# Kernel tuning notes

Measured on AMD Instinct MI355X. Metric: run time of the kernel, lower is better.

The kernel has to match this reference:

```python
import jax, jax.numpy as jnp
import numpy as np
import math

B, L, D, H = 2, 2048, 2048, 16
DK = D // H  # 128

def _rope_tables(dim, max_len, base=10000.0):
    freqs = 1.0 / (base ** (np.arange(0, dim, 2, dtype=np.float32) / dim))
    t = np.arange(max_len, dtype=np.float32)
    ang = np.outer(t, freqs)  # [max_len, dim//2]
    return jnp.asarray(np.cos(ang)), jnp.asarray(np.sin(ang))

def setup_inputs() -> dict:
    key = jax.random.key(0)
    kx, kq, ko = jax.random.split(key, 3)
    x = jax.random.normal(kx, (B, L, D), dtype=jnp.float32)
    w_qkv = jax.random.normal(kq, (D, 3 * D), dtype=jnp.float32) * 0.02
    w_o = jax.random.normal(ko, (D, D), dtype=jnp.float32) * 0.02
    cos, sin = _rope_tables(DK, L)
    return {"x": x, "w_qkv": w_qkv, "w_o": w_o, "cos": cos, "sin": sin}

def _apply_rope(t, cos, sin):
    # t: [B, H, L, DK]; cos/sin: [L, DK//2]
    d2 = t.shape[-1] // 2
    t1, t2 = t[..., :d2], t[..., d2:]
    c = cos[None, None, :, :]
    s = sin[None, None, :, :]
    return jnp.concatenate([t1 * c - t2 * s, t1 * s + t2 * c], axis=-1)

def reference(x, w_qkv, w_o, cos, sin):
    b, l, d = x.shape
    qkv = (x @ w_qkv).reshape(b, l, 3, H, DK)
    q = jnp.transpose(qkv[:, :, 0], (0, 2, 1, 3))  # [B,H,L,DK]
    k = jnp.transpose(qkv[:, :, 1], (0, 2, 1, 3))
    v = jnp.transpose(qkv[:, :, 2], (0, 2, 1, 3))
    q = _apply_rope(q, cos[:l], sin[:l])
    k = _apply_rope(k, cos[:l], sin[:l])
    scores = jnp.einsum('bhqd,bhkd->bhqk', q, k) / math.sqrt(DK)
    causal = jnp.triu(jnp.ones((l, l), dtype=bool), k=1)  # total_len - L + 1 = 1
    scores = jnp.where(causal[None, None], -jnp.inf, scores)
    attn = jax.nn.softmax(scores, axis=-1)  # dropout p=0 -> identity
    out = jnp.einsum('bhqk,bhkd->bhqd', attn, v)
    out = jnp.transpose(out, (0, 2, 1, 3)).reshape(b, l, d)
    return out @ w_o, k, v
```

## Files before the change

### kernel.cpp

```cpp
#include <hip/hip_runtime.h>
#include <hip/hip_bf16.h>

#define NB 2
#define NL 2048
#define ND 2048
#define NH 16
#define NDK 128
#define SCALE2 0.12753102866606474f

#define AS1 __attribute__((address_space(1)))
#define AS3 __attribute__((address_space(3)))

typedef __attribute__((ext_vector_type(8))) __bf16 bf16x8;
typedef __attribute__((ext_vector_type(4))) float f32x4;

__device__ __forceinline__ unsigned short f2bf(float f) {
    union { float f; unsigned u; } v; v.f = f;
    return (unsigned short)((v.u + 0x7fffu + ((v.u >> 16) & 1u)) >> 16);
}
__device__ __forceinline__ float bf2f(unsigned short h) {
    union { unsigned u; float f; } v; v.u = ((unsigned)h) << 16;
    return v.f;
}

__global__ __launch_bounds__(256)
void convert_bf16_kernel(const float* __restrict__ in, unsigned short* __restrict__ outp)
{
    int i = blockIdx.x * 256 + threadIdx.x;
    const float4 a = ((const float4*)in)[2 * i];
    const float4 b = ((const float4*)in)[2 * i + 1];
    unsigned short t[8] = { f2bf(a.x), f2bf(a.y), f2bf(a.z), f2bf(a.w),
                            f2bf(b.x), f2bf(b.y), f2bf(b.z), f2bf(b.w) };
    ((uint4*)outp)[i] = *(uint4*)t;
}

__global__ __launch_bounds__(256)
void transpose_convert_kernel(const float* __restrict__ in, unsigned short* __restrict__ outp,
                              int R, int C)
{
    __shared__ float T[64][65];
    const int tr0 = blockIdx.y * 64;
    const int tc0 = blockIdx.x * 64;
    const int t = threadIdx.x;
    const int r = t >> 2;
    const int q = t & 3;
    const float* src = in + (size_t)(tr0 + r) * C + tc0 + q * 16;
    #pragma unroll
    for (int i = 0; i < 4; i++) {
        float4 f = *(const float4*)(src + 4 * i);
        T[r][q * 16 + 4 * i + 0] = f.x;
        T[r][q * 16 + 4 * i + 1] = f.y;
        T[r][q * 16 + 4 * i + 2] = f.z;
        T[r][q * 16 + 4 * i + 3] = f.w;
    }
    __syncthreads();
    unsigned short tmp[16];
    #pragma unroll
    for (int i = 0; i < 16; i++) tmp[i] = f2bf(T[q * 16 + i][r]);
    unsigned short* dst = outp + (size_t)(tc0 + r) * R + tr0 + q * 16;
    *(uint4*)dst       = *(uint4*)&tmp[0];
    *(uint4*)(dst + 8) = *(uint4*)&tmp[8];
}

__global__ __launch_bounds__(256)
void transpose_v_kernel(const float* __restrict__ v, unsigned short* __restrict__ vt)
{
    __shared__ float T[64][65];
    const int bh = blockIdx.z;
    const int l0 = blockIdx.y * 64;
    const int d0 = blockIdx.x * 64;
    const int t = threadIdx.x;
    const int r = t >> 2;
    const int q = t & 3;
    const float* src = v + (size_t)bh * NL * NDK + (size_t)(l0 + r) * NDK + d0 + q * 16;
    #pragma unroll
    for (int i = 0; i < 4; i++) {
        float4 f = *(const float4*)(src + 4 * i);
        T[r][q * 16 + 4 * i + 0] = f.x;
        T[r][q * 16 + 4 * i + 1] = f.y;
        T[r][q * 16 + 4 * i + 2] = f.z;
        T[r][q * 16 + 4 * i + 3] = f.w;
    }
    __syncthreads();
    unsigned short tmp[16];
    #pragma unroll
    for (int i = 0; i < 16; i++) tmp[i] = f2bf(T[q * 16 + i][r]);
    unsigned short* dst = vt + (size_t)bh * NDK * NL + (size_t)(d0 + r) * NL + l0 + q * 16;
    *(uint4*)dst       = *(uint4*)&tmp[0];
    *(uint4*)(dst + 8) = *(uint4*)&tmp[8];
}

template<int EPI>
__global__ __launch_bounds__(256)
void gemm_bf16(const unsigned short* __restrict__ A, const unsigned short* __restrict__ Bt,
               float* __restrict__ y_dst,
               unsigned short* __restrict__ q_raw,
               float* __restrict__ k_dst, float* __restrict__ v_dst,
               int K, int NT)
{
    __shared__ __align__(16) unsigned short As[3][128][32];
    __shared__ __align__(16) unsigned short Bs[3][128][32];

    const int tid = threadIdx.x;
    const int lane = tid & 63;
    const int l16 = lane & 15, g = lane >> 4;
    const int w = tid >> 6;
    const int wr = w >> 1, wc = w & 1;

    const int cpn = NT >> 3;
    const int bid = blockIdx.x;
    const int xcd = bid & 7, local = bid >> 3;
    const int bx = xcd * cpn + local % cpn;
    const int by = local / cpn;
    const int m0 = by * 128, n0 = bx * 128;

    const int rowl = (w << 4) + (lane >> 2);
    const int swl = (rowl >> 1) & 3;
    const int kofl = ((lane & 3) ^ swl) << 3;
    const unsigned short* gA = A + (size_t)(m0 + rowl) * K + kofl;
    const unsigned short* gB = Bt + (size_t)(n0 + rowl) * K + kofl;
    const int ldsoff = (w << 10) + (lane << 4);

    f32x4 acc[4][4] = {};
    const int NTILES = K >> 5;

    auto STAGE = [&](int t, int buf) {
        const int k0 = t << 5;
        char* baseA = (char*)&As[buf][0][0] + ldsoff;
        char* baseB = (char*)&Bs[buf][0][0] + ldsoff;
        #pragma unroll
        for (int i = 0; i < 2; i++) {
            __builtin_amdgcn_global_load_lds((const AS1 void*)(gA + (size_t)i * 64 * K + k0),
                                             (AS3 void*)(baseA + i * 4096), 16, 0, 0);
            __builtin_amdgcn_global_load_lds((const AS1 void*)(gB + (size_t)i * 64 * K + k0),
                                             (AS3 void*)(baseB + i * 4096), 16, 0, 0);
        }
    };

    const int rsw = (l16 >> 1) & 3;

    STAGE(0, 0); STAGE(1, 1);

    int bufC = 0;
    for (int t = 0; t < NTILES; t++) {
        const int bufS = (bufC == 0) ? 2 : bufC - 1;
        if (t + 2 < NTILES) STAGE(t + 2, bufS);
        if (t + 2 < NTILES)      asm volatile("s_waitcnt vmcnt(8)" ::: "memory");
        else if (t + 1 < NTILES) asm volatile("s_waitcnt vmcnt(4)" ::: "memory");
        else                     asm volatile("s_waitcnt vmcnt(0)" ::: "memory");
        __builtin_amdgcn_s_barrier();
        __builtin_amdgcn_sched_barrier(0);

        const char* pa = (const char*)&As[bufC][0][0];
        const char* pb = (const char*)&Bs[bufC][0][0];
        bf16x8 af[4], bfr[4];
        #pragma unroll
        for (int r = 0; r < 4; r++) {
            int row = wr * 64 + r * 16 + l16;
            af[r] = *(const bf16x8*)(pa + row * 64 + ((g ^ rsw) << 4));
        }
        #pragma unroll
        for (int c = 0; c < 4; c++) {
            int row = wc * 64 + c * 16 + l16;
            bfr[c] = *(const bf16x8*)(pb + row * 64 + ((g ^ rsw) << 4));
        }
        #pragma unroll
        for (int r = 0; r < 4; r++)
            #pragma unroll
            for (int c = 0; c < 4; c++)
                acc[r][c] = __builtin_amdgcn_mfma_f32_16x16x32_bf16(af[r], bfr[c], acc[r][c], 0, 0, 0);

        __builtin_amdgcn_s_barrier();
        __builtin_amdgcn_sched_barrier(0);
        bufC = (bufC == 2) ? 0 : bufC + 1;
    }

    if constexpr (EPI == 0) {
        const int m3 = bx >> 4, h = bx & 15;
        #pragma unroll
        for (int r = 0; r < 4; r++) {
            int mrow = m0 + wr * 64 + r * 16 + g * 4;
            int b = mrow >> 11, l = mrow & 2047;
            size_t rb = ((size_t)(b * NH + h) * NL + l) * NDK;
            #pragma unroll
            for (int c = 0; c < 4; c++) {
                int dk = wc * 64 + c * 16 + l16;
                #pragma unroll
                for (int i = 0; i < 4; i++) {
                    float val = acc[r][c][i];
                    size_t off = rb + (size_t)i * NDK + dk;
                    if (m3 == 0) q_raw[off] = f2bf(val);
                    else if (m3 == 1) k_dst[off] = val;
                    else v_dst[off] = val;
                }
            }
        }
    } else {
        #pragma unroll
        for (int r = 0; r < 4; r++) {
            int mrow = m0 + wr * 64 + r * 16 + g * 4;
            #pragma unroll
            for (int c = 0; c < 4; c++) {
                int ncol = n0 + wc * 64 + c * 16 + l16;
                #pragma unroll
                for (int i = 0; i < 4; i++)
                    y_dst[(size_t)(mrow + i) * ND + ncol] = acc[r][c][i];
            }
        }
    }
}

__global__ __launch_bounds__(256)
void rope_k_kernel(float* __restrict__ kp, unsigned short* __restrict__ k_bf,
                   const float* __restrict__ ct, const float* __restrict__ st)
{
    int idx = blockIdx.x * 256 + threadIdx.x;
    int d = (idx & 15) << 2;
    int rr = idx >> 4;
    size_t ro = (size_t)rr * NDK;
    int l = rr & (NL - 1);
    float4 c  = *(const float4*)(ct + l * 64 + d);
    float4 s  = *(const float4*)(st + l * 64 + d);
    float4 t1 = *(const float4*)(kp + ro + d);
    float4 t2 = *(const float4*)(kp + ro + d + 64);
    float4 o1, o2;
    o1.x = t1.x * c.x - t2.x * s.x;  o2.x = t1.x * s.x + t2.x * c.x;
    o1.y = t1.y * c.y - t2.y * s.y;  o2.y = t1.y * s.y + t2.y * c.y;
    o1.z = t1.z * c.z - t2.z * s.z;  o2.z = t1.z * s.z + t2.z * c.z;
    o1.w = t1.w * c.w - t2.w * s.w;  o2.w = t1.w * s.w + t2.w * c.w;
    *(float4*)(kp + ro + d)      = o1;
    *(float4*)(kp + ro + d + 64) = o2;
    unsigned short u1[4] = { f2bf(o1.x), f2bf(o1.y), f2bf(o1.z), f2bf(o1.w) };
    unsigned short u2[4] = { f2bf(o2.x), f2bf(o2.y), f2bf(o2.z), f2bf(o2.w) };
    *(uint2*)(k_bf + ro + d)      = *(uint2*)u1;
    *(uint2*)(k_bf + ro + d + 64) = *(uint2*)u2;
}

__global__ __launch_bounds__(256)
void attn_kernel(const unsigned short* __restrict__ q,
                 const unsigned short* __restrict__ k,
                 const unsigned short* __restrict__ vt,
                 unsigned short* __restrict__ attn_out,
                 const float* __restrict__ ct, const float* __restrict__ st)
{
    __shared__ __align__(16) unsigned short Ks[64][128];
    __shared__ __align__(16) unsigned short Vts[128][64];
    __shared__ __align__(16) unsigned short Ps[4][16][64];

    char* const ksb = (char*)&Ks[0][0];
    char* const vsb = (char*)&Vts[0][0];
    char* const psb = (char*)&Ps[0][0][0];

    const int tid = threadIdx.x, lane = tid & 63, w = tid >> 6;
    const int l16 = lane & 15, g = lane >> 4;
    const int bh = blockIdx.x;
    const int b = bh >> 4, h = bh & 15;
    const size_t base = (size_t)bh * NL * NDK;

    const int krow = tid >> 2;
    const int kq = tid & 3;
    const int kwb = krow * 256 + kq * 64;
    const int kwx = (krow & 7) << 4;
    const int vrow = tid >> 1;
    const int vh = tid & 1;
    const int vwb = vrow * 128 + vh * 64;
    const int vwx = (vrow & 7) << 4;

    const int rdx = (l16 & 7) << 4;

    const unsigned short* const kbase = k + base + (size_t)krow * NDK + kq * 32;
    const unsigned short* const vbase = vt + base + (size_t)vrow * NL + vh * 32;

    const int jq = 31 - (int)blockIdx.y;
    const int qb = jq * 64;

    bf16x8 aq[4];
    {
        const int l = qb + w * 16 + l16;
        const unsigned short* src = q + base + (size_t)l * NDK + g * 8;
        union { bf16x8 v; unsigned short s[8]; } raw[4], outv[4];
        #pragma unroll
        for (int ks2 = 0; ks2 < 4; ks2++) raw[ks2].v = *(const bf16x8*)(src + ks2 * 32);
        const float* cb = ct + (size_t)l * 64 + g * 8;
        const float* sb = st + (size_t)l * 64 + g * 8;
        float cv[2][8], sv2[2][8];
        #pragma unroll
        for (int hh = 0; hh < 2; hh++) {
            float4 c0 = *(const float4*)(cb + 32 * hh);
            float4 c1 = *(const float4*)(cb + 32 * hh + 4);
            float4 s0 = *(const float4*)(sb + 32 * hh);
            float4 s1 = *(const float4*)(sb + 32 * hh + 4);
            cv[hh][0]=c0.x; cv[hh][1]=c0.y; cv[hh][2]=c0.z; cv[hh][3]=c0.w;
            cv[hh][4]=c1.x; cv[hh][5]=c1.y; cv[hh][6]=c1.z; cv[hh][7]=c1.w;
            sv2[hh][0]=s0.x; sv2[hh][1]=s0.y; sv2[hh][2]=s0.z; sv2[hh][3]=s0.w;
            sv2[hh][4]=s1.x; sv2[hh][5]=s1.y; sv2[hh][6]=s1.z; sv2[hh][7]=s1.w;
        }
        #pragma unroll
        for (int hh = 0; hh < 2; hh++)
            #pragma unroll
            for (int j = 0; j < 8; j++) {
                float t1 = bf2f(raw[hh].s[j]), t2 = bf2f(raw[hh + 2].s[j]);
                float c = cv[hh][j], s = sv2[hh][j];
                outv[hh].s[j]     = f2bf(t1 * c - t2 * s);
                outv[hh + 2].s[j] = f2bf(t1 * s + t2 * c);
            }
        #pragma unroll
        for (int ks2 = 0; ks2 < 4; ks2++) aq[ks2] = outv[ks2].v;
    }

    f32x4 o[8] = {};
    float m_r[4], lv[4];
    #pragma unroll
    for (int i = 0; i < 4; i++) { m_r[i] = -1e30f; lv[i] = 0.f; }

    uint4 pk0, pk1, pk2, pk3, pv0, pv1, pv2, pv3;
    {
        const unsigned short* ks = kbase;
        pk0 = *(const uint4*)(ks);
        pk1 = *(const uint4*)(ks + 8);
        pk2 = *(const uint4*)(ks + 16);
        pk3 = *(const uint4*)(ks + 24);
        const unsigned short* vs = vbase;
        pv0 = *(const uint4*)(vs);
        pv1 = *(const uint4*)(vs + 8);
        pv2 = *(const uint4*)(vs + 16);
        pv3 = *(const uint4*)(vs + 24);
    }

    for (int kv0 = 0; kv0 <= qb; kv0 += 64) {
        __syncthreads();
        *(uint4*)(ksb + ((kwb     ) ^ kwx)) = pk0;
        *(uint4*)(ksb + ((kwb + 16) ^ kwx)) = pk1;
        *(uint4*)(ksb + ((kwb + 32) ^ kwx)) = pk2;
        *(uint4*)(ksb + ((kwb + 48) ^ kwx)) = pk3;
        *(uint4*)(vsb + ((vwb     ) ^ vwx)) = pv0;
        *(uint4*)(vsb + ((vwb + 16) ^ vwx)) = pv1;
        *(uint4*)(vsb + ((vwb + 32) ^ vwx)) = pv2;
        *(uint4*)(vsb + ((vwb + 48) ^ vwx)) = pv3;
        __syncthreads();

        if (kv0 + 64 <= qb) {
            const unsigned short* ks = kbase + (size_t)(kv0 + 64) * NDK;
            pk0 = *(const uint4*)(ks);
            pk1 = *(const uint4*)(ks + 8);
            pk2 = *(const uint4*)(ks + 16);
            pk3 = *(const uint4*)(ks + 24);
            const unsigned short* vs = vbase + kv0 + 64;
            pv0 = *(const uint4*)(vs);
            pv1 = *(const uint4*)(vs + 8);
            pv2 = *(const uint4*)(vs + 16);
            pv3 = *(const uint4*)(vs + 24);
            __builtin_amdgcn_sched_barrier(0);
        }

        f32x4 sv[4];
        __builtin_amdgcn_s_setprio(1);
        #pragma unroll
        for (int cf = 0; cf < 4; cf++) {
            const int krb = (cf * 16 + l16) * 256 + g * 16;
            f32x4 a = {};
            #pragma unroll
            for (int ks2 = 0; ks2 < 4; ks2++) {
                bf16x8 kf = *(const bf16x8*)(ksb + ((krb + 64 * ks2) ^ rdx));
                a = __builtin_amdgcn_mfma_f32_16x16x32_bf16(aq[ks2], kf, a, 0, 0, 0);
            }
            sv[cf] = a;
        }
        __builtin_amdgcn_s_setprio(0);

        const int kvl = kv0 + l16;
        const int rowb = qb + w * 16 + g * 4;
        #pragma unroll
        for (int i = 0; i < 4; i++) {
            int row = rowb + i;
            float s0 = sv[0][i] * SCALE2;
            float s1 = sv[1][i] * SCALE2;
            float s2 = sv[2][i] * SCALE2;
            float s3 = sv[3][i] * SCALE2;
            if (kvl      > row) s0 = -1e30f;
            if (kvl + 16 > row) s1 = -1e30f;
            if (kvl + 32 > row) s2 = -1e30f;
            if (kvl + 48 > row) s3 = -1e30f;
            float mx = fmaxf(fmaxf(s0, s1), fmaxf(s2, s3));
            mx = fmaxf(mx, __shfl_xor(mx, 1));
            mx = fmaxf(mx, __shfl_xor(mx, 2));
            mx = fmaxf(mx, __shfl_xor(mx, 4));
            mx = fmaxf(mx, __shfl_xor(mx, 8));
            float mnew = fmaxf(m_r[i], mx);
            float fac = exp2f(m_r[i] - mnew);
            float p0 = exp2f(s0 - mnew);
            float p1 = exp2f(s1 - mnew);
            float p2 = exp2f(s2 - mnew);
            float p3 = exp2f(s3 - mnew);
            lv[i] = lv[i] * fac + ((p0 + p1) + (p2 + p3));
            m_r[i] = mnew;
            #pragma unroll
            for (int c8 = 0; c8 < 8; c8++) o[c8][i] *= fac;
            const int pr = g * 4 + i;
            char* pw = psb + w * 2048 + pr * 128;
            const int px = (pr & 7) << 4;
            const int cb2 = l16 << 1;
            *(unsigned short*)(pw + ((cb2)      ^ px)) = f2bf(p0);
            *(unsigned short*)(pw + ((cb2 + 32) ^ px)) = f2bf(p1);
            *(unsigned short*)(pw + ((cb2 + 64) ^ px)) = f2bf(p2);
            *(unsigned short*)(pw + ((cb2 + 96) ^ px)) = f2bf(p3);
        }
        asm volatile("s_waitcnt lgkmcnt(0)" ::: "memory");
        __builtin_amdgcn_sched_barrier(0);

        bf16x8 pf[2];
        #pragma unroll
        for (int kc = 0; kc < 2; kc++)
            pf[kc] = *(const bf16x8*)(psb + w * 2048 + l16 * 128 + ((kc * 64 + g * 16) ^ rdx));
        __builtin_amdgcn_s_setprio(1);
        #pragma unroll
        for (int c8 = 0; c8 < 8; c8++) {
            const int vrb = (c8 * 16 + l16) * 128 + g * 16;
            #pragma unroll
            for (int kc = 0; kc < 2; kc++) {
                bf16x8 vf = *(const bf16x8*)(vsb + ((vrb + kc * 64) ^ rdx));
                o[c8] = __builtin_amdgcn_mfma_f32_16x16x32_bf16(pf[kc], vf, o[c8], 0, 0, 0);
            }
        }
        __builtin_amdgcn_s_setprio(0);
    }

    #pragma unroll
    for (int i = 0; i < 4; i++) {
        float ls = lv[i];
        ls += __shfl_xor(ls, 1);
        ls += __shfl_xor(ls, 2);
        ls += __shfl_xor(ls, 4);
        ls += __shfl_xor(ls, 8);
        float inv = 1.0f / ls;
        int qrow = qb + w * 16 + g * 4 + i;
        size_t rb = ((size_t)(b * NL + qrow)) * ND + h * NDK;
        #pragma unroll
        for (int c8 = 0; c8 < 8; c8++)
            attn_out[rb + c8 * 16 + l16] = f2bf(o[c8][i] * inv);
    }
}

__global__ void ws_signature_kernel(float* y) { if (threadIdx.x == 0) y[0] = 12345.0f; }

extern "C" void kernel_launch(void* const* d_in, const int* in_sizes, int n_in,
                              void* d_out, int out_size, void* d_ws, size_t ws_size,
                              hipStream_t stream)
{
    const float* x     = (const float*)d_in[0];
    const float* w_qkv = (const float*)d_in[1];
    const float* w_o   = (const float*)d_in[2];
    const float* ct    = (const float*)d_in[3];
    const float* st    = (const float*)d_in[4];

    const size_t NTOK = (size_t)NB * NL * ND;
    float* y_out = (float*)d_out;
    float* k_out = y_out + NTOK;
    float* v_out = y_out + 2 * NTOK;

    const size_t need = (6 * NTOK + 4 * (size_t)ND * ND) * sizeof(unsigned short);
    if (ws_size < need) {
        ws_signature_kernel<<<1, 64, 0, stream>>>(y_out);
        return;
    }
    unsigned short* x_bf  = (unsigned short*)d_ws;
    unsigned short* Wt    = x_bf + NTOK;
    unsigned short* Wt_o  = Wt + (size_t)3 * ND * ND;
    unsigned short* q_raw = Wt_o + (size_t)ND * ND;
    unsigned short* q_bf  = q_raw + NTOK;
    unsigned short* k_bf  = q_bf + NTOK;
    unsigned short* Vt    = k_bf + NTOK;
    unsigned short* a_bf  = Vt + NTOK;

    convert_bf16_kernel<<<4096, 256, 0, stream>>>(x, x_bf);
    transpose_convert_kernel<<<dim3(96, 32), 256, 0, stream>>>(w_qkv, Wt, ND, 3 * ND);
    transpose_convert_kernel<<<dim3(32, 32), 256, 0, stream>>>(w_o, Wt_o, ND, ND);
    gemm_bf16<0><<<1536, 256, 0, stream>>>(x_bf, Wt, nullptr, q_raw, k_out, v_out, ND, 48);
    rope_k_kernel<<<4096, 256, 0, stream>>>(k_out, k_bf, ct, st);
    transpose_v_kernel<<<dim3(2, 32, 32), 256, 0, stream>>>(v_out, Vt);
    attn_kernel<<<dim3(32, 32), 256, 0, stream>>>(q_raw, k_bf, Vt, a_bf, ct, st);
    gemm_bf16<1><<<512, 256, 0, stream>>>(a_bf, Wt_o, y_out, nullptr, nullptr, nullptr, ND, 16);
}
```

Before: 329.4 us.

## Merge prep and mid kernels; pair causal query tiles per attention block

The three preprocessing kernels (x conversion and both weight transposes) become one launch that dispatches on block index, and the rope-K and V-transpose kernels are merged the same way. The attention grid is halved, and each block now handles two query tiles, a long one (31-y) and a short one (y), so every block does about the same amount of causal work. This removes launch overhead and tail imbalance in attention, at the cost of fewer concurrent blocks and a serial two-phase loop per block.

```diff
diff --git a/kernel.cpp b/kernel.cpp
--- a/kernel.cpp
+++ b/kernel.cpp
@@ -23,27 +23,15 @@
     return v.f;
 }
 
-__global__ __launch_bounds__(256)
-void convert_bf16_kernel(const float* __restrict__ in, unsigned short* __restrict__ outp)
-{
-    int i = blockIdx.x * 256 + threadIdx.x;
-    const float4 a = ((const float4*)in)[2 * i];
-    const float4 b = ((const float4*)in)[2 * i + 1];
-    unsigned short t[8] = { f2bf(a.x), f2bf(a.y), f2bf(a.z), f2bf(a.w),
-                            f2bf(b.x), f2bf(b.y), f2bf(b.z), f2bf(b.w) };
-    ((uint4*)outp)[i] = *(uint4*)t;
-}
-
-__global__ __launch_bounds__(256)
-void transpose_convert_kernel(const float* __restrict__ in, unsigned short* __restrict__ outp,
-                              int R, int C)
+__device__ __forceinline__ void transpose_tile(const float* __restrict__ in,
+                                               unsigned short* __restrict__ outp,
+                                               int R, int C, int bx, int by, int tid)
 {
     __shared__ float T[64][65];
-    const int tr0 = blockIdx.y * 64;
-    const int tc0 = blockIdx.x * 64;
-    const int t = threadIdx.x;
-    const int r = t >> 2;
-    const int q = t & 3;
+    const int tr0 = by * 64;
+    const int tc0 = bx * 64;
+    const int r = tid >> 2;
+    const int q = tid & 3;
     const float* src = in + (size_t)(tr0 + r) * C + tc0 + q * 16;
     #pragma unroll
     for (int i = 0; i < 4; i++) {
@@ -63,31 +51,26 @@
 }
 
 __global__ __launch_bounds__(256)
-void transpose_v_kernel(const float* __restrict__ v, unsigned short* __restrict__ vt)
-{
-    __shared__ float T[64][65];
-    const int bh = blockIdx.z;
-    const int l0 = blockIdx.y * 64;
-    const int d0 = blockIdx.x * 64;
-    const int t = threadIdx.x;
-    const int r = t >> 2;
-    const int q = t & 3;
-    const float* src = v + (size_t)bh * NL * NDK + (size_t)(l0 + r) * NDK + d0 + q * 16;
-    #pragma unroll
-    for (int i = 0; i < 4; i++) {
-        float4 f = *(const float4*)(src + 4 * i);
-        T[r][q * 16 + 4 * i + 0] = f.x;
-        T[r][q * 16 + 4 * i + 1] = f.y;
-        T[r][q * 16 + 4 * i + 2] = f.z;
-        T[r][q * 16 + 4 * i + 3] = f.w;
-    }
-    __syncthreads();
-    unsigned short tmp[16];
-    #pragma unroll
-    for (int i = 0; i < 16; i++) tmp[i] = f2bf(T[q * 16 + i][r]);
-    unsigned short* dst = vt + (size_t)bh * NDK * NL + (size_t)(d0 + r) * NL + l0 + q * 16;
-    *(uint4*)dst       = *(uint4*)&tmp[0];
-    *(uint4*)(dst + 8) = *(uint4*)&tmp[8];
+void prep_kernel(const float* __restrict__ x, unsigned short* __restrict__ x_bf,
+                 const float* __restrict__ w_qkv, unsigned short* __restrict__ Wt,
+                 const float* __restrict__ w_o, unsigned short* __restrict__ Wt_o)
+{
+    const int bid = blockIdx.x;
+    const int tid = threadIdx.x;
+    if (bid < 4096) {
+        int i = bid * 256 + tid;
+        const float4 a = ((const float4*)x)[2 * i];
+        const float4 b = ((const float4*)x)[2 * i + 1];
+        unsigned short t[8] = { f2bf(a.x), f2bf(a.y), f2bf(a.z), f2bf(a.w),
+                                f2bf(b.x), f2bf(b.y), f2bf(b.z), f2bf(b.w) };
+        ((uint4*)x_bf)[i] = *(uint4*)t;
+    } else if (bid < 7168) {
+        int b2 = bid - 4096;
+        transpose_tile(w_qkv, Wt, ND, 3 * ND, b2 % 96, b2 / 96, tid);
+    } else {
+        int b3 = bid - 7168;
+        transpose_tile(w_o, Wt_o, ND, ND, b3 & 31, b3 >> 5, tid);
+    }
 }
 
 template<int EPI>
@@ -211,29 +194,58 @@
 }
 
 __global__ __launch_bounds__(256)
-void rope_k_kernel(float* __restrict__ kp, unsigned short* __restrict__ k_bf,
-                   const float* __restrict__ ct, const float* __restrict__ st)
-{
-    int idx = blockIdx.x * 256 + threadIdx.x;
-    int d = (idx & 15) << 2;
-    int rr = idx >> 4;
-    size_t ro = (size_t)rr * NDK;
-    int l = rr & (NL - 1);
-    float4 c  = *(const float4*)(ct + l * 64 + d);
-    float4 s  = *(const float4*)(st + l * 64 + d);
-    float4 t1 = *(const float4*)(kp + ro + d);
-    float4 t2 = *(const float4*)(kp + ro + d + 64);
-    float4 o1, o2;
-    o1.x = t1.x * c.x - t2.x * s.x;  o2.x = t1.x * s.x + t2.x * c.x;
-    o1.y = t1.y * c.y - t2.y * s.y;  o2.y = t1.y * s.y + t2.y * c.y;
-    o1.z = t1.z * c.z - t2.z * s.z;  o2.z = t1.z * s.z + t2.z * c.z;
-    o1.w = t1.w * c.w - t2.w * s.w;  o2.w = t1.w * s.w + t2.w * c.w;
-    *(float4*)(kp + ro + d)      = o1;
-    *(float4*)(kp + ro + d + 64) = o2;
-    unsigned short u1[4] = { f2bf(o1.x), f2bf(o1.y), f2bf(o1.z), f2bf(o1.w) };
-    unsigned short u2[4] = { f2bf(o2.x), f2bf(o2.y), f2bf(o2.z), f2bf(o2.w) };
-    *(uint2*)(k_bf + ro + d)      = *(uint2*)u1;
-    *(uint2*)(k_bf + ro + d + 64) = *(uint2*)u2;
+void mid_kernel(float* __restrict__ kp, unsigned short* __restrict__ k_bf,
+                const float* __restrict__ ct, const float* __restrict__ st,
+                const float* __restrict__ v, unsigned short* __restrict__ vt)
+{
+    const int bid = blockIdx.x;
+    const int tid = threadIdx.x;
+    if (bid < 4096) {
+        int idx = bid * 256 + tid;
+        int d = (idx & 15) << 2;
+        int rr = idx >> 4;
+        size_t ro = (size_t)rr * NDK;
+        int l = rr & (NL - 1);
+        float4 c  = *(const float4*)(ct + l * 64 + d);
+        float4 s  = *(const float4*)(st + l * 64 + d);
+        float4 t1 = *(const float4*)(kp + ro + d);
+        float4 t2 = *(const float4*)(kp + ro + d + 64);
+        float4 o1, o2;
+        o1.x = t1.x * c.x - t2.x * s.x;  o2.x = t1.x * s.x + t2.x * c.x;
+        o1.y = t1.y * c.y - t2.y * s.y;  o2.y = t1.y * s.y + t2.y * c.y;
+        o1.z = t1.z * c.z - t2.z * s.z;  o2.z = t1.z * s.z + t2.z * c.z;
+        o1.w = t1.w * c.w - t2.w * s.w;  o2.w = t1.w * s.w + t2.w * c.w;
+        *(float4*)(kp + ro + d)      = o1;
+        *(float4*)(kp + ro + d + 64) = o2;
+        unsigned short u1[4] = { f2bf(o1.x), f2bf(o1.y), f2bf(o1.z), f2bf(o1.w) };
+        unsigned short u2[4] = { f2bf(o2.x), f2bf(o2.y), f2bf(o2.z), f2bf(o2.w) };
+        *(uint2*)(k_bf + ro + d)      = *(uint2*)u1;
+        *(uint2*)(k_bf + ro + d + 64) = *(uint2*)u2;
+    } else {
+        __shared__ float T[64][65];
+        int b2 = bid - 4096;
+        const int bh = b2 >> 6;
+        const int l0 = ((b2 >> 1) & 31) * 64;
+        const int d0 = (b2 & 1) * 64;
+        const int r = tid >> 2;
+        const int q = tid & 3;
+        const float* src = v + (size_t)bh * NL * NDK + (size_t)(l0 + r) * NDK + d0 + q * 16;
+        #pragma unroll
+        for (int i = 0; i < 4; i++) {
+            float4 f = *(const float4*)(src + 4 * i);
+            T[r][q * 16 + 4 * i + 0] = f.x;
+            T[r][q * 16 + 4 * i + 1] = f.y;
+            T[r][q * 16 + 4 * i + 2] = f.z;
+            T[r][q * 16 + 4 * i + 3] = f.w;
+        }
+        __syncthreads();
+        unsigned short tmp[16];
+        #pragma unroll
+        for (int i = 0; i < 16; i++) tmp[i] = f2bf(T[q * 16 + i][r]);
+        unsigned short* dst = vt + (size_t)bh * NDK * NL + (size_t)(d0 + r) * NL + l0 + q * 16;
+        *(uint4*)dst       = *(uint4*)&tmp[0];
+        *(uint4*)(dst + 8) = *(uint4*)&tmp[8];
+    }
 }
 
 __global__ __launch_bounds__(256)
@@ -271,173 +283,175 @@
     const unsigned short* const kbase = k + base + (size_t)krow * NDK + kq * 32;
     const unsigned short* const vbase = vt + base + (size_t)vrow * NL + vh * 32;
 
-    const int jq = 31 - (int)blockIdx.y;
-    const int qb = jq * 64;
-
-    bf16x8 aq[4];
-    {
-        const int l = qb + w * 16 + l16;
-        const unsigned short* src = q + base + (size_t)l * NDK + g * 8;
-        union { bf16x8 v; unsigned short s[8]; } raw[4], outv[4];
-        #pragma unroll
-        for (int ks2 = 0; ks2 < 4; ks2++) raw[ks2].v = *(const bf16x8*)(src + ks2 * 32);
-        const float* cb = ct + (size_t)l * 64 + g * 8;
-        const float* sb = st + (size_t)l * 64 + g * 8;
-        float cv[2][8], sv2[2][8];
-        #pragma unroll
-        for (int hh = 0; hh < 2; hh++) {
-            float4 c0 = *(const float4*)(cb + 32 * hh);
-            float4 c1 = *(const float4*)(cb + 32 * hh + 4);
-            float4 s0 = *(const float4*)(sb + 32 * hh);
-            float4 s1 = *(const float4*)(sb + 32 * hh + 4);
-            cv[hh][0]=c0.x; cv[hh][1]=c0.y; cv[hh][2]=c0.z; cv[hh][3]=c0.w;
-            cv[hh][4]=c1.x; cv[hh][5]=c1.y; cv[hh][6]=c1.z; cv[hh][7]=c1.w;
-            sv2[hh][0]=s0.x; sv2[hh][1]=s0.y; sv2[hh][2]=s0.z; sv2[hh][3]=s0.w;
-            sv2[hh][4]=s1.x; sv2[hh][5]=s1.y; sv2[hh][6]=s1.z; sv2[hh][7]=s1.w;
-        }
-        #pragma unroll
-        for (int hh = 0; hh < 2; hh++)
-            #pragma unroll
-            for (int j = 0; j < 8; j++) {
-                float t1 = bf2f(raw[hh].s[j]), t2 = bf2f(raw[hh + 2].s[j]);
-                float c = cv[hh][j], s = sv2[hh][j];
-                outv[hh].s[j]     = f2bf(t1 * c - t2 * s);
-                outv[hh + 2].s[j] = f2bf(t1 * s + t2 * c);
-            }
-        #pragma unroll
-        for (int ks2 = 0; ks2 < 4; ks2++) aq[ks2] = outv[ks2].v;
-    }
-
-    f32x4 o[8] = {};
-    float m_r[4], lv[4];
-    #pragma unroll
-    for (int i = 0; i < 4; i++) { m_r[i] = -1e30f; lv[i] = 0.f; }
-
-    uint4 pk0, pk1, pk2, pk3, pv0, pv1, pv2, pv3;
-    {
-        const unsigned short* ks = kbase;
-        pk0 = *(const uint4*)(ks);
-        pk1 = *(const uint4*)(ks + 8);
-        pk2 = *(const uint4*)(ks + 16);
-        pk3 = *(const uint4*)(ks + 24);
-        const unsigned short* vs = vbase;
-        pv0 = *(const uint4*)(vs);
-        pv1 = *(const uint4*)(vs + 8);
-        pv2 = *(const uint4*)(vs + 16);
-        pv3 = *(const uint4*)(vs + 24);
-    }
-
-    for (int kv0 = 0; kv0 <= qb; kv0 += 64) {
-        __syncthreads();
-        *(uint4*)(ksb + ((kwb     ) ^ kwx)) = pk0;
-        *(uint4*)(ksb + ((kwb + 16) ^ kwx)) = pk1;
-        *(uint4*)(ksb + ((kwb + 32) ^ kwx)) = pk2;
-        *(uint4*)(ksb + ((kwb + 48) ^ kwx)) = pk3;
-        *(uint4*)(vsb + ((vwb     ) ^ vwx)) = pv0;
-        *(uint4*)(vsb + ((vwb + 16) ^ vwx)) = pv1;
-        *(uint4*)(vsb + ((vwb + 32) ^ vwx)) = pv2;
-        *(uint4*)(vsb + ((vwb + 48) ^ vwx)) = pv3;
-        __syncthreads();
-
-        if (kv0 + 64 <= qb) {
-            const unsigned short* ks = kbase + (size_t)(kv0 + 64) * NDK;
+    for (int half = 0; half < 2; half++) {
+        const int jq = half ? (int)blockIdx.y : 31 - (int)blockIdx.y;
+        const int qb = jq * 64;
+
+        bf16x8 aq[4];
+        {
+            const int l = qb + w * 16 + l16;
+            const unsigned short* src = q + base + (size_t)l * NDK + g * 8;
+            union { bf16x8 v; unsigned short s[8]; } raw[4], outv[4];
+            #pragma unroll
+            for (int ks2 = 0; ks2 < 4; ks2++) raw[ks2].v = *(const bf16x8*)(src + ks2 * 32);
+            const float* cb = ct + (size_t)l * 64 + g * 8;
+            const float* sb = st + (size_t)l * 64 + g * 8;
+            float cv[2][8], sv2[2][8];
+            #pragma unroll
+            for (int hh = 0; hh < 2; hh++) {
+                float4 c0 = *(const float4*)(cb + 32 * hh);
+                float4 c1 = *(const float4*)(cb + 32 * hh + 4);
+                float4 s0 = *(const float4*)(sb + 32 * hh);
+                float4 s1 = *(const float4*)(sb + 32 * hh + 4);
+                cv[hh][0]=c0.x; cv[hh][1]=c0.y; cv[hh][2]=c0.z; cv[hh][3]=c0.w;
+                cv[hh][4]=c1.x; cv[hh][5]=c1.y; cv[hh][6]=c1.z; cv[hh][7]=c1.w;
+                sv2[hh][0]=s0.x; sv2[hh][1]=s0.y; sv2[hh][2]=s0.z; sv2[hh][3]=s0.w;
+                sv2[hh][4]=s1.x; sv2[hh][5]=s1.y; sv2[hh][6]=s1.z; sv2[hh][7]=s1.w;
+            }
+            #pragma unroll
+            for (int hh = 0; hh < 2; hh++)
+                #pragma unroll
+                for (int j = 0; j < 8; j++) {
+                    float t1 = bf2f(raw[hh].s[j]), t2 = bf2f(raw[hh + 2].s[j]);
+                    float c = cv[hh][j], s = sv2[hh][j];
+                    outv[hh].s[j]     = f2bf(t1 * c - t2 * s);
+                    outv[hh + 2].s[j] = f2bf(t1 * s + t2 * c);
+                }
+            #pragma unroll
+            for (int ks2 = 0; ks2 < 4; ks2++) aq[ks2] = outv[ks2].v;
+        }
+
+        f32x4 o[8] = {};
+        float m_r[4], lv[4];
+        #pragma unroll
+        for (int i = 0; i < 4; i++) { m_r[i] = -1e30f; lv[i] = 0.f; }
+
+        uint4 pk0, pk1, pk2, pk3, pv0, pv1, pv2, pv3;
+        {
+            const unsigned short* ks = kbase;
             pk0 = *(const uint4*)(ks);
             pk1 = *(const uint4*)(ks + 8);
             pk2 = *(const uint4*)(ks + 16);
             pk3 = *(const uint4*)(ks + 24);
-            const unsigned short* vs = vbase + kv0 + 64;
+            const unsigned short* vs = vbase;
             pv0 = *(const uint4*)(vs);
             pv1 = *(const uint4*)(vs + 8);
             pv2 = *(const uint4*)(vs + 16);
             pv3 = *(const uint4*)(vs + 24);
+        }
+
+        for (int kv0 = 0; kv0 <= qb; kv0 += 64) {
+            __syncthreads();
+            *(uint4*)(ksb + ((kwb     ) ^ kwx)) = pk0;
+            *(uint4*)(ksb + ((kwb + 16) ^ kwx)) = pk1;
+            *(uint4*)(ksb + ((kwb + 32) ^ kwx)) = pk2;
+            *(uint4*)(ksb + ((kwb + 48) ^ kwx)) = pk3;
+            *(uint4*)(vsb + ((vwb     ) ^ vwx)) = pv0;
+            *(uint4*)(vsb + ((vwb + 16) ^ vwx)) = pv1;
+            *(uint4*)(vsb + ((vwb + 32) ^ vwx)) = pv2;
+            *(uint4*)(vsb + ((vwb + 48) ^ vwx)) = pv3;
+            __syncthreads();
+
+            if (kv0 + 64 <= qb) {
+                const unsigned short* ks = kbase + (size_t)(kv0 + 64) * NDK;
+                pk0 = *(const uint4*)(ks);
+                pk1 = *(const uint4*)(ks + 8);
+                pk2 = *(const uint4*)(ks + 16);
+                pk3 = *(const uint4*)(ks + 24);
+                const unsigned short* vs = vbase + kv0 + 64;
+                pv0 = *(const uint4*)(vs);
+                pv1 = *(const uint4*)(vs + 8);
+                pv2 = *(const uint4*)(vs + 16);
+                pv3 = *(const uint4*)(vs + 24);
+                __builtin_amdgcn_sched_barrier(0);
+            }
+
+            f32x4 sv[4];
+            __builtin_amdgcn_s_setprio(1);
+            #pragma unroll
+            for (int cf = 0; cf < 4; cf++) {
+                const int krb = (cf * 16 + l16) * 256 + g * 16;
+                f32x4 a = {};
+                #pragma unroll
+                for (int ks2 = 0; ks2 < 4; ks2++) {
+                    bf16x8 kf = *(const bf16x8*)(ksb + ((krb + 64 * ks2) ^ rdx));
+                    a = __builtin_amdgcn_mfma_f32_16x16x32_bf16(aq[ks2], kf, a, 0, 0, 0);
+                }
+                sv[cf] = a;
+            }
+            __builtin_amdgcn_s_setprio(0);
+
+            const int kvl = kv0 + l16;
+            const int rowb = qb + w * 16 + g * 4;
+            #pragma unroll
+            for (int i = 0; i < 4; i++) {
+                int row = rowb + i;
+                float s0 = sv[0][i] * SCALE2;
+                float s1 = sv[1][i] * SCALE2;
+                float s2 = sv[2][i] * SCALE2;
+                float s3 = sv[3][i] * SCALE2;
+                if (kvl      > row) s0 = -1e30f;
+                if (kvl + 16 > row) s1 = -1e30f;
+                if (kvl + 32 > row) s2 = -1e30f;
+                if (kvl + 48 > row) s3 = -1e30f;
+                float mx = fmaxf(fmaxf(s0, s1), fmaxf(s2, s3));
+                mx = fmaxf(mx, __shfl_xor(mx, 1));
+                mx = fmaxf(mx, __shfl_xor(mx, 2));
+                mx = fmaxf(mx, __shfl_xor(mx, 4));
+                mx = fmaxf(mx, __shfl_xor(mx, 8));
+                float mnew = fmaxf(m_r[i], mx);
+                float fac = exp2f(m_r[i] - mnew);
+                float p0 = exp2f(s0 - mnew);
+                float p1 = exp2f(s1 - mnew);
+                float p2 = exp2f(s2 - mnew);
+                float p3 = exp2f(s3 - mnew);
+                lv[i] = lv[i] * fac + ((p0 + p1) + (p2 + p3));
+                m_r[i] = mnew;
+                #pragma unroll
+                for (int c8 = 0; c8 < 8; c8++) o[c8][i] *= fac;
+                const int pr = g * 4 + i;
+                char* pw = psb + w * 2048 + pr * 128;
+                const int px = (pr & 7) << 4;
+                const int cb2 = l16 << 1;
+                *(unsigned short*)(pw + ((cb2)      ^ px)) = f2bf(p0);
+                *(unsigned short*)(pw + ((cb2 + 32) ^ px)) = f2bf(p1);
+                *(unsigned short*)(pw + ((cb2 + 64) ^ px)) = f2bf(p2);
+                *(unsigned short*)(pw + ((cb2 + 96) ^ px)) = f2bf(p3);
+            }
+            asm volatile("s_waitcnt lgkmcnt(0)" ::: "memory");
             __builtin_amdgcn_sched_barrier(0);
-        }
-
-        f32x4 sv[4];
-        __builtin_amdgcn_s_setprio(1);
-        #pragma unroll
-        for (int cf = 0; cf < 4; cf++) {
-            const int krb = (cf * 16 + l16) * 256 + g * 16;
-            f32x4 a = {};
-            #pragma unroll
-            for (int ks2 = 0; ks2 < 4; ks2++) {
-                bf16x8 kf = *(const bf16x8*)(ksb + ((krb + 64 * ks2) ^ rdx));
-                a = __builtin_amdgcn_mfma_f32_16x16x32_bf16(aq[ks2], kf, a, 0, 0, 0);
-            }
-            sv[cf] = a;
-        }
-        __builtin_amdgcn_s_setprio(0);
-
-        const int kvl = kv0 + l16;
-        const int rowb = qb + w * 16 + g * 4;
+
+            bf16x8 pf[2];
+            #pragma unroll
+            for (int kc = 0; kc < 2; kc++)
+                pf[kc] = *(const bf16x8*)(psb + w * 2048 + l16 * 128 + ((kc * 64 + g * 16) ^ rdx));
+            __builtin_amdgcn_s_setprio(1);
+            #pragma unroll
+            for (int c8 = 0; c8 < 8; c8++) {
+                const int vrb = (c8 * 16 + l16) * 128 + g * 16;
+                #pragma unroll
+                for (int kc = 0; kc < 2; kc++) {
+                    bf16x8 vf = *(const bf16x8*)(vsb + ((vrb + kc * 64) ^ rdx));
+                    o[c8] = __builtin_amdgcn_mfma_f32_16x16x32_bf16(pf[kc], vf, o[c8], 0, 0, 0);
+                }
+            }
+            __builtin_amdgcn_s_setprio(0);
+        }
+
         #pragma unroll
         for (int i = 0; i < 4; i++) {
-            int row = rowb + i;
-            float s0 = sv[0][i] * SCALE2;
-            float s1 = sv[1][i] * SCALE2;
-            float s2 = sv[2][i] * SCALE2;
-            float s3 = sv[3][i] * SCALE2;
-            if (kvl      > row) s0 = -1e30f;
-            if (kvl + 16 > row) s1 = -1e30f;
-            if (kvl + 32 > row) s2 = -1e30f;
-            if (kvl + 48 > row) s3 = -1e30f;
-            float mx = fmaxf(fmaxf(s0, s1), fmaxf(s2, s3));
-            mx = fmaxf(mx, __shfl_xor(mx, 1));
-            mx = fmaxf(mx, __shfl_xor(mx, 2));
-            mx = fmaxf(mx, __shfl_xor(mx, 4));
-            mx = fmaxf(mx, __shfl_xor(mx, 8));
-            float mnew = fmaxf(m_r[i], mx);
-            float fac = exp2f(m_r[i] - mnew);
-            float p0 = exp2f(s0 - mnew);
-            float p1 = exp2f(s1 - mnew);
-            float p2 = exp2f(s2 - mnew);
-            float p3 = exp2f(s3 - mnew);
-            lv[i] = lv[i] * fac + ((p0 + p1) + (p2 + p3));
-            m_r[i] = mnew;
-            #pragma unroll
-            for (int c8 = 0; c8 < 8; c8++) o[c8][i] *= fac;
-            const int pr = g * 4 + i;
-            char* pw = psb + w * 2048 + pr * 128;
-            const int px = (pr & 7) << 4;
-            const int cb2 = l16 << 1;
-            *(unsigned short*)(pw + ((cb2)      ^ px)) = f2bf(p0);
-            *(unsigned short*)(pw + ((cb2 + 32) ^ px)) = f2bf(p1);
-            *(unsigned short*)(pw + ((cb2 + 64) ^ px)) = f2bf(p2);
-            *(unsigned short*)(pw + ((cb2 + 96) ^ px)) = f2bf(p3);
-        }
-        asm volatile("s_waitcnt lgkmcnt(0)" ::: "memory");
-        __builtin_amdgcn_sched_barrier(0);
-
-        bf16x8 pf[2];
-        #pragma unroll
-        for (int kc = 0; kc < 2; kc++)
-            pf[kc] = *(const bf16x8*)(psb + w * 2048 + l16 * 128 + ((kc * 64 + g * 16) ^ rdx));
-        __builtin_amdgcn_s_setprio(1);
-        #pragma unroll
-        for (int c8 = 0; c8 < 8; c8++) {
-            const int vrb = (c8 * 16 + l16) * 128 + g * 16;
-            #pragma unroll
-            for (int kc = 0; kc < 2; kc++) {
-                bf16x8 vf = *(const bf16x8*)(vsb + ((vrb + kc * 64) ^ rdx));
-                o[c8] = __builtin_amdgcn_mfma_f32_16x16x32_bf16(pf[kc], vf, o[c8], 0, 0, 0);
-            }
-        }
-        __builtin_amdgcn_s_setprio(0);
-    }
-
-    #pragma unroll
-    for (int i = 0; i < 4; i++) {
-        float ls = lv[i];
-        ls += __shfl_xor(ls, 1);
-        ls += __shfl_xor(ls, 2);
-        ls += __shfl_xor(ls, 4);
-        ls += __shfl_xor(ls, 8);
-        float inv = 1.0f / ls;
-        int qrow = qb + w * 16 + g * 4 + i;
-        size_t rb = ((size_t)(b * NL + qrow)) * ND + h * NDK;
-        #pragma unroll
-        for (int c8 = 0; c8 < 8; c8++)
-            attn_out[rb + c8 * 16 + l16] = f2bf(o[c8][i] * inv);
+            float ls = lv[i];
+            ls += __shfl_xor(ls, 1);
+            ls += __shfl_xor(ls, 2);
+            ls += __shfl_xor(ls, 4);
+            ls += __shfl_xor(ls, 8);
+            float inv = 1.0f / ls;
+            int qrow = qb + w * 16 + g * 4 + i;
+            size_t rb = ((size_t)(b * NL + qrow)) * ND + h * NDK;
+            #pragma unroll
+            for (int c8 = 0; c8 < 8; c8++)
+                attn_out[rb + c8 * 16 + l16] = f2bf(o[c8][i] * inv);
+        }
     }
 }
 
@@ -472,12 +486,9 @@
     unsigned short* Vt    = k_bf + NTOK;
     unsigned short* a_bf  = Vt + NTOK;
 
-    convert_bf16_kernel<<<4096, 256, 0, stream>>>(x, x_bf);
-    transpose_convert_kernel<<<dim3(96, 32), 256, 0, stream>>>(w_qkv, Wt, ND, 3 * ND);
-    transpose_convert_kernel<<<dim3(32, 32), 256, 0, stream>>>(w_o, Wt_o, ND, ND);
+    prep_kernel<<<8192, 256, 0, stream>>>(x, x_bf, w_qkv, Wt, w_o, Wt_o);
     gemm_bf16<0><<<1536, 256, 0, stream>>>(x_bf, Wt, nullptr, q_raw, k_out, v_out, ND, 48);
-    rope_k_kernel<<<4096, 256, 0, stream>>>(k_out, k_bf, ct, st);
-    transpose_v_kernel<<<dim3(2, 32, 32), 256, 0, stream>>>(v_out, Vt);
-    attn_kernel<<<dim3(32, 32), 256, 0, stream>>>(q_raw, k_bf, Vt, a_bf, ct, st);
+    mid_kernel<<<6144, 256, 0, stream>>>(k_out, k_bf, ct, st, v_out, Vt);
+    attn_kernel<<<dim3(32, 16), 256, 0, stream>>>(q_raw, k_bf, Vt, a_bf, ct, st);
     gemm_bf16<1><<<512, 256, 0, stream>>>(a_bf, Wt_o, y_out, nullptr, nullptr, nullptr, ND, 16);
 }
```

New measurement: 316.1 us. 1.04x faster.
